# Kernel optimization log

Hardware: AMD Instinct MI355X
Metric: run time of the kernel (lower is better)

Reference implementation:

```python
import jax, jax.numpy as jnp
import numpy as np

N_NODES = 100000
N_EDGES = 1600000
IN_DIM, HID_DIM, OUT_DIM = 128, 128, 64


def setup_inputs() -> dict:
    key = jax.random.key(0)
    ks = jax.random.split(key, 5)
    x = jax.random.normal(ks[0], (N_NODES, IN_DIM), dtype=jnp.float32)
    edge_index = jax.random.randint(ks[1], (2, N_EDGES), 0, N_NODES, dtype=jnp.int64)
    W1 = jax.random.normal(ks[2], (IN_DIM, HID_DIM), dtype=jnp.float32) * (1.0 / np.sqrt(IN_DIM))
    b1 = jnp.zeros((HID_DIM,), dtype=jnp.float32)
    W2 = jax.random.normal(ks[3], (HID_DIM, OUT_DIM), dtype=jnp.float32) * (1.0 / np.sqrt(HID_DIM))
    b2 = jnp.zeros((OUT_DIM,), dtype=jnp.float32)
    return {"x": x, "edge_index": edge_index, "W1": W1, "b1": b1, "W2": W2, "b2": b2}


def _gcn_conv(h, row, col, norm, b, n_nodes):
    # h: [N, F] already linearly transformed; message = norm_e * h[src]; scatter-add to dst
    msg = h[row] * norm[:, None]                      # [E+N, F]
    out = jax.ops.segment_sum(msg, col, num_segments=n_nodes)
    return out + b


def reference(x, edge_index, W1, b1, W2, b2):
    n = x.shape[0]
    loops = jnp.arange(n, dtype=edge_index.dtype)
    row = jnp.concatenate([edge_index[0], loops])     # sources (incl. self loops)
    col = jnp.concatenate([edge_index[1], loops])     # targets
    # symmetric normalization: deg over targets with unit edge weights
    deg = jax.ops.segment_sum(jnp.ones_like(col, dtype=x.dtype), col, num_segments=n)
    dinv = jnp.where(deg > 0, jax.lax.rsqrt(jnp.maximum(deg, 1.0)), 0.0)
    norm = dinv[row] * dinv[col]                      # [E+N]
    h = jax.nn.relu(_gcn_conv(x @ W1, row, col, norm, b1, n))
    out = _gcn_conv(h @ W2, row, col, norm, b2, n)
    return out.mean(axis=0)                           # [OUT_DIM]
```

## Files before the change

### kernel.cpp

```cpp
#include <hip/hip_runtime.h>

#define N_NODES 100000
#define N_EDGES 1600000
#define IN_DIM 128
#define HID_DIM 128
#define OUT_DIM 64
#define BKT_SHIFT 8
#define BKT_SIZE 256
#define NBKT ((N_NODES + BKT_SIZE - 1) / BKT_SIZE)
#define B1 256
#define HIST_N (NBKT * B1)
#define HIST_N2 (2 * HIST_N)
#define GEMM_BLKS ((N_NODES + 127) / 128)

typedef float v2f __attribute__((ext_vector_type(2)));
typedef float v4f __attribute__((ext_vector_type(4)));
typedef short v8s __attribute__((ext_vector_type(8)));

__device__ __forceinline__ unsigned int f2bf(float f) {
  unsigned int u = __float_as_uint(f);
  return (u + 0x7FFFu + ((u >> 16) & 1u)) >> 16;
}

__device__ __forceinline__ void load4(const void* ei, int is64, int half, int base,
                                      int* v) {
  if (is64) {
    const long long* e = (const long long*)ei + (size_t)half * N_EDGES + base;
    longlong2 a = *(const longlong2*)e;
    longlong2 b = *(const longlong2*)(e + 2);
    v[0] = (int)a.x; v[1] = (int)a.y; v[2] = (int)b.x; v[3] = (int)b.y;
  } else {
    const int* e = (const int*)ei + (size_t)half * N_EDGES + base;
    int4 a = *(const int4*)e;
    v[0] = a.x; v[1] = a.y; v[2] = a.z; v[3] = a.w;
  }
}

__device__ __forceinline__ int detect64_block(const unsigned int* ei, int* sh) {
  if (threadIdx.x == 0) *sh = 0;
  __syncthreads();
  if (ei[1 + 2 * threadIdx.x] != 0u) *sh = 1;
  __syncthreads();
  return (*sh == 0) ? 1 : 0;
}

__global__ __launch_bounds__(256) void front_kernel(const float* __restrict__ x,
                                                    const float* __restrict__ W,
                                                    const void* ei,
                                                    unsigned int* __restrict__ G,
                                                    int* hist, float* S) {
  __shared__ __align__(16) char smem[2 * 128 * 136 * 2];
  if (blockIdx.x >= GEMM_BLKS) {
    int* hd = (int*)smem;
    int* hs = hd + NBKT;
    int* sh = hs + NBKT;
    const int hb = blockIdx.x - GEMM_BLKS;
    if (hb == 0 && threadIdx.x < HID_DIM) S[threadIdx.x] = 0.f;
    const int is64 = detect64_block((const unsigned int*)ei, sh);
    for (int k = threadIdx.x; k < NBKT; k += 256) { hd[k] = 0; hs[k] = 0; }
    __syncthreads();
    for (int g = hb * 256 + threadIdx.x; g < N_EDGES / 4; g += B1 * 256) {
      int r[4], c[4];
      load4(ei, is64, 0, g * 4, r);
      load4(ei, is64, 1, g * 4, c);
#pragma unroll
      for (int k = 0; k < 4; k++) {
        atomicAdd(&hd[c[k] >> BKT_SHIFT], 1);
        atomicAdd(&hs[r[k] >> BKT_SHIFT], 1);
      }
    }
    __syncthreads();
    for (int k = threadIdx.x; k < NBKT; k += 256) {
      hist[k * B1 + hb] = hd[k];
      hist[HIST_N + k * B1 + hb] = hs[k];
    }
    return;
  }
  typedef unsigned short us_row[136];
  us_row* lx = (us_row*)smem;
  us_row* lwt = (us_row*)(smem + 128 * 136 * 2);
  const int t = threadIdx.x;
  const int row0 = blockIdx.x * 128;

  {
    const float4* W4 = (const float4*)W;
    for (int it = 0; it < 16; ++it) {
      int idx = t + 256 * it;
      int k = idx >> 5, c4 = (idx & 31) * 4;
      float4 w = W4[idx];
      lwt[c4 + 0][k] = (unsigned short)f2bf(w.x);
      lwt[c4 + 1][k] = (unsigned short)f2bf(w.y);
      lwt[c4 + 2][k] = (unsigned short)f2bf(w.z);
      lwt[c4 + 3][k] = (unsigned short)f2bf(w.w);
    }
  }
  {
    const float4* x4 = (const float4*)(x + (size_t)row0 * IN_DIM);
    for (int it = 0; it < 16; ++it) {
      int idx = t + 256 * it;
      int r = idx >> 5, kq = (idx & 31) * 4;
      float4 v = make_float4(0.f, 0.f, 0.f, 0.f);
      if (row0 + r < N_NODES) v = x4[idx];
      unsigned int p0 = (f2bf(v.y) << 16) | f2bf(v.x);
      unsigned int p1 = (f2bf(v.w) << 16) | f2bf(v.z);
      *(uint2*)&lx[r][kq] = make_uint2(p0, p1);
    }
  }
  __syncthreads();

  const int lane = t & 63;
  const int wv = t >> 6;
  const int m0 = wv * 32;
  const int lrow = lane & 15;
  const int lk = (lane >> 4) * 8;

  v4f acc[2][8];
#pragma unroll
  for (int si = 0; si < 2; si++)
#pragma unroll
    for (int n = 0; n < 8; n++) acc[si][n] = (v4f){0.f, 0.f, 0.f, 0.f};

#pragma unroll
  for (int kk = 0; kk < 128; kk += 32) {
    v8s a0 = *(const v8s*)&lx[m0 + lrow][kk + lk];
    v8s a1 = *(const v8s*)&lx[m0 + 16 + lrow][kk + lk];
#pragma unroll
    for (int n = 0; n < 8; n++) {
      v8s b = *(const v8s*)&lwt[n * 16 + lrow][kk + lk];
      acc[0][n] = __builtin_amdgcn_mfma_f32_16x16x32_bf16(a0, b, acc[0][n], 0, 0, 0);
      acc[1][n] = __builtin_amdgcn_mfma_f32_16x16x32_bf16(a1, b, acc[1][n], 0, 0, 0);
    }
  }

  unsigned char* G8 = (unsigned char*)G;
#pragma unroll
  for (int si = 0; si < 2; si++)
#pragma unroll
    for (int n = 0; n < 8; n++) {
      int colg = n * 16 + (lane & 15);
#pragma unroll
      for (int i = 0; i < 4; i++) {
        int r = row0 + m0 + si * 16 + (lane >> 4) * 4 + i;
        if (r < N_NODES) {
          float v = acc[si][n][i];
          int pk = __builtin_amdgcn_cvt_pk_fp8_f32(v, v, 0, false);
          G8[(size_t)r * HID_DIM + colg] = (unsigned char)(pk & 0xFF);
        }
      }
    }
}

__global__ void scan1_kernel(int* arr, int* bsum, int n) {
  __shared__ int tmp[256];
  int i = blockIdx.x * 256 + threadIdx.x;
  int v = (i < n) ? arr[i] : 0;
  tmp[threadIdx.x] = v;
  __syncthreads();
  for (int off = 1; off < 256; off <<= 1) {
    int t2 = (threadIdx.x >= off) ? tmp[threadIdx.x - off] : 0;
    __syncthreads();
    tmp[threadIdx.x] += t2;
    __syncthreads();
  }
  if (i < n) arr[i] = tmp[threadIdx.x] - v;
  if (threadIdx.x == 255) bsum[blockIdx.x] = tmp[255];
}

__global__ void scan2_kernel(int* bsum, int nb) {
  __shared__ int tmp[1024];
  int v = (threadIdx.x < nb) ? bsum[threadIdx.x] : 0;
  tmp[threadIdx.x] = v;
  __syncthreads();
  for (int off = 1; off < 1024; off <<= 1) {
    int t2 = (threadIdx.x >= off) ? tmp[threadIdx.x - off] : 0;
    __syncthreads();
    tmp[threadIdx.x] += t2;
    __syncthreads();
  }
  if (threadIdx.x < nb) bsum[threadIdx.x] = tmp[threadIdx.x] - v;
}

__global__ __launch_bounds__(256) void scatter_kernel(const void* ei, const int* hist,
                                                      const int* bsum,
                                                      unsigned int* pairs) {
  __shared__ int cd[NBKT], cs[NBKT], sh[1];
  const int is64 = detect64_block((const unsigned int*)ei, sh);
  for (int k = threadIdx.x; k < NBKT; k += 256) {
    cd[k] = hist[k * B1 + blockIdx.x] + bsum[k];
    cs[k] = hist[HIST_N + k * B1 + blockIdx.x] + bsum[NBKT + k];
  }
  __syncthreads();
  for (int g = blockIdx.x * 256 + threadIdx.x; g < N_EDGES / 4; g += B1 * 256) {
    int r[4], c[4];
    load4(ei, is64, 0, g * 4, r);
    load4(ei, is64, 1, g * 4, c);
#pragma unroll
    for (int k = 0; k < 4; k++) {
      int pd = atomicAdd(&cd[c[k] >> BKT_SHIFT], 1);
      pairs[pd] = ((unsigned int)(c[k] & (BKT_SIZE - 1)) << 17) | (unsigned int)r[k];
      int ps = atomicAdd(&cs[r[k] >> BKT_SHIFT], 1);
      pairs[ps] = ((unsigned int)(r[k] & (BKT_SIZE - 1)) << 17) | (unsigned int)c[k];
    }
  }
}

__global__ __launch_bounds__(256) void csr_kernel(const int* hist, const int* bsum,
                                                  const unsigned int* pairs,
                                                  int* rowptr, int* csr, float* dinv) {
  __shared__ int cnt[BKT_SIZE], sc[BKT_SIZE], cur[BKT_SIZE];
  const int k = blockIdx.x;
  const int base = hist[k * B1] + bsum[k];
  const int end = (k == NBKT - 1) ? N_EDGES : hist[(k + 1) * B1] + bsum[k + 1];
  const int nseg = end - base;
  const int l = threadIdx.x;
  cnt[l] = 0;
  __syncthreads();
  for (int i = l; i < nseg; i += 256) atomicAdd(&cnt[pairs[base + i] >> 17], 1);
  __syncthreads();
  sc[l] = cnt[l];
  __syncthreads();
  for (int off = 1; off < BKT_SIZE; off <<= 1) {
    int v = (l >= off) ? sc[l - off] : 0;
    __syncthreads();
    sc[l] += v;
    __syncthreads();
  }
  {
    int excl = sc[l] - cnt[l];
    cur[l] = base + excl;
    int v = k * BKT_SIZE + l;
    if (v < N_NODES) {
      rowptr[v] = base + excl;
      dinv[v] = rsqrtf((float)(cnt[l] + 1));
    }
  }
  if (k == NBKT - 1 && l == 0) rowptr[N_NODES] = N_EDGES;
  __syncthreads();
  for (int i = l; i < nseg; i += 256) {
    unsigned int pk = pairs[base + i];
    int pos = atomicAdd(&cur[pk >> 17], 1);
    csr[pos] = (int)(pk & 0x1FFFFu);
  }
}

__global__ __launch_bounds__(256) void outsum_kernel(const int* hist, const int* bsum,
                                                     const unsigned int* pairs,
                                                     const float* __restrict__ dinv,
                                                     float* wacc) {
  __shared__ float fb[BKT_SIZE];
  const int k = blockIdx.x;
  const int base = hist[HIST_N + k * B1] + bsum[NBKT + k];
  const int end =
      (k == NBKT - 1) ? 2 * N_EDGES : hist[HIST_N + (k + 1) * B1] + bsum[NBKT + k + 1];
  fb[threadIdx.x] = 0.f;
  __syncthreads();
  for (int i = base + threadIdx.x; i < end; i += 256) {
    unsigned int pk = pairs[i];
    atomicAdd(&fb[pk >> 17], dinv[pk & 0x1FFFFu]);
  }
  __syncthreads();
  int v = k * BKT_SIZE + threadIdx.x;
  if (v < N_NODES) wacc[v] = fb[threadIdx.x];
}

__global__ __launch_bounds__(256) void aggregate_kernel(
    const unsigned int* __restrict__ G, const int* __restrict__ rowptr,
    const int* __restrict__ csr, const float* __restrict__ dinv,
    const float* __restrict__ wacc, const float* __restrict__ b1,
    float* __restrict__ S) {
  const int lane = threadIdx.x & 63;
  const int sub = lane & 31;
  const int half = lane >> 5;
  const int wid = blockIdx.x * (blockDim.x >> 6) + (threadIdx.x >> 6);
  const int nwaves = gridDim.x * (blockDim.x >> 6);
  const float4 b = ((const float4*)b1)[sub];
  v2f s01 = {0.f, 0.f}, s23 = {0.f, 0.f};

  for (int c = wid; c < N_NODES; c += nwaves) {
    const int start = rowptr[c];
    const int cnum = rowptr[c + 1] - start;
    float d = 0.f;
    v2f a01 = {0.f, 0.f}, a23 = {0.f, 0.f};
    if (half == 0) {
      d = dinv[c];
      unsigned int g = G[c * 32 + sub];
      a01 = __builtin_amdgcn_cvt_pk_f32_fp8((int)g, false) * d;
      a23 = __builtin_amdgcn_cvt_pk_f32_fp8((int)g, true) * d;
    }
    for (int j0 = 0; j0 < cnum; j0 += 64) {
      int src = 0;
      float dvl = 0.f;
      if (j0 + lane < cnum) {
        src = __builtin_nontemporal_load(&csr[start + j0 + lane]);
        dvl = dinv[src];
      }
      const int m = min(64, cnum - j0);
      int i = 0;
      for (; i + 16 <= m; i += 16) {
        int s0 = __shfl(src, i + half);
        int s1 = __shfl(src, i + 2 + half);
        int s2 = __shfl(src, i + 4 + half);
        int s3 = __shfl(src, i + 6 + half);
        int s4 = __shfl(src, i + 8 + half);
        int s5 = __shfl(src, i + 10 + half);
        int s6 = __shfl(src, i + 12 + half);
        int s7 = __shfl(src, i + 14 + half);
        float w0 = __shfl(dvl, i + half);
        float w1 = __shfl(dvl, i + 2 + half);
        float w2 = __shfl(dvl, i + 4 + half);
        float w3 = __shfl(dvl, i + 6 + half);
        float w4 = __shfl(dvl, i + 8 + half);
        float w5 = __shfl(dvl, i + 10 + half);
        float w6 = __shfl(dvl, i + 12 + half);
        float w7 = __shfl(dvl, i + 14 + half);
        unsigned int g0 = G[s0 * 32 + sub];
        unsigned int g1 = G[s1 * 32 + sub];
        unsigned int g2 = G[s2 * 32 + sub];
        unsigned int g3 = G[s3 * 32 + sub];
        unsigned int g4 = G[s4 * 32 + sub];
        unsigned int g5 = G[s5 * 32 + sub];
        unsigned int g6 = G[s6 * 32 + sub];
        unsigned int g7 = G[s7 * 32 + sub];
        a01 += __builtin_amdgcn_cvt_pk_f32_fp8((int)g0, false) * w0;
        a23 += __builtin_amdgcn_cvt_pk_f32_fp8((int)g0, true) * w0;
        a01 += __builtin_amdgcn_cvt_pk_f32_fp8((int)g1, false) * w1;
        a23 += __builtin_amdgcn_cvt_pk_f32_fp8((int)g1, true) * w1;
        a01 += __builtin_amdgcn_cvt_pk_f32_fp8((int)g2, false) * w2;
        a23 += __builtin_amdgcn_cvt_pk_f32_fp8((int)g2, true) * w2;
        a01 += __builtin_amdgcn_cvt_pk_f32_fp8((int)g3, false) * w3;
        a23 += __builtin_amdgcn_cvt_pk_f32_fp8((int)g3, true) * w3;
        a01 += __builtin_amdgcn_cvt_pk_f32_fp8((int)g4, false) * w4;
        a23 += __builtin_amdgcn_cvt_pk_f32_fp8((int)g4, true) * w4;
        a01 += __builtin_amdgcn_cvt_pk_f32_fp8((int)g5, false) * w5;
        a23 += __builtin_amdgcn_cvt_pk_f32_fp8((int)g5, true) * w5;
        a01 += __builtin_amdgcn_cvt_pk_f32_fp8((int)g6, false) * w6;
        a23 += __builtin_amdgcn_cvt_pk_f32_fp8((int)g6, true) * w6;
        a01 += __builtin_amdgcn_cvt_pk_f32_fp8((int)g7, false) * w7;
        a23 += __builtin_amdgcn_cvt_pk_f32_fp8((int)g7, true) * w7;
      }
      for (; i + 2 <= m; i += 2) {
        int s = __shfl(src, i + half);
        float w = __shfl(dvl, i + half);
        unsigned int g = G[s * 32 + sub];
        a01 += __builtin_amdgcn_cvt_pk_f32_fp8((int)g, false) * w;
        a23 += __builtin_amdgcn_cvt_pk_f32_fp8((int)g, true) * w;
      }
      if (i < m) {
        int s = __shfl(src, i);
        float w = __shfl(dvl, i);
        if (half == 0) {
          unsigned int g = G[s * 32 + sub];
          a01 += __builtin_amdgcn_cvt_pk_f32_fp8((int)g, false) * w;
          a23 += __builtin_amdgcn_cvt_pk_f32_fp8((int)g, true) * w;
        }
      }
    }
    a01.x += __shfl(a01.x, sub + 32);
    a01.y += __shfl(a01.y, sub + 32);
    a23.x += __shfl(a23.x, sub + 32);
    a23.y += __shfl(a23.y, sub + 32);
    if (half == 0) {
      float wc = d * (wacc[c] + d);
      s01.x += wc * fmaxf(fmaf(d, a01.x, b.x), 0.f);
      s01.y += wc * fmaxf(fmaf(d, a01.y, b.y), 0.f);
      s23.x += wc * fmaxf(fmaf(d, a23.x, b.z), 0.f);
      s23.y += wc * fmaxf(fmaf(d, a23.y, b.w), 0.f);
    }
  }

  __shared__ float ls[HID_DIM];
  if (threadIdx.x < HID_DIM) ls[threadIdx.x] = 0.f;
  __syncthreads();
  if (half == 0) {
    atomicAdd(&ls[4 * sub + 0], s01.x);
    atomicAdd(&ls[4 * sub + 1], s01.y);
    atomicAdd(&ls[4 * sub + 2], s23.x);
    atomicAdd(&ls[4 * sub + 3], s23.y);
  }
  __syncthreads();
  if (threadIdx.x < HID_DIM) atomicAdd(&S[threadIdx.x], ls[threadIdx.x]);
}

__global__ void finish_kernel(const float* __restrict__ S, const float* __restrict__ W2,
                              const float* __restrict__ b2, float* __restrict__ out) {
  int j = threadIdx.x;
  float acc = 0.f;
  for (int k = 0; k < HID_DIM; k++) acc += S[k] * W2[k * OUT_DIM + j];
  out[j] = acc * (1.0f / N_NODES) + b2[j];
}

extern "C" void kernel_launch(void* const* d_in, const int* in_sizes, int n_in,
                              void* d_out, int out_size, void* d_ws, size_t ws_size,
                              hipStream_t stream) {
  const float* x  = (const float*)d_in[0];
  const void*  ei = d_in[1];
  const float* W1 = (const float*)d_in[2];
  const float* b1 = (const float*)d_in[3];
  const float* W2 = (const float*)d_in[4];
  const float* b2 = (const float*)d_in[5];
  float* out = (float*)d_out;

  char* p = (char*)d_ws;
  size_t off = 0;
  auto alloc = [&](size_t bytes) -> void* {
    void* r = p + off;
    off = (off + bytes + 63) & ~(size_t)63;
    return r;
  };
  int*   hist   = (int*)alloc((size_t)HIST_N2 * 4);
  int*   bsum   = (int*)alloc(1024 * 4);
  unsigned int* pairs = (unsigned int*)alloc((size_t)2 * N_EDGES * 4);
  int*   rowptr = (int*)alloc(((size_t)N_NODES + 1) * 4);
  int*   csr    = (int*)alloc((size_t)N_EDGES * 4);
  float* dinv   = (float*)alloc((size_t)N_NODES * 4);
  float* wacc   = (float*)alloc((size_t)N_NODES * 4);
  float* S      = (float*)alloc(HID_DIM * 4);
  unsigned int* G = (unsigned int*)alloc((size_t)N_NODES * HID_DIM);
  (void)ws_size; (void)n_in; (void)in_sizes; (void)out_size;

  const int NBH = HIST_N2 / 256;

  front_kernel<<<GEMM_BLKS + B1, 256, 0, stream>>>(x, W1, ei, G, hist, S);
  scan1_kernel<<<NBH, 256, 0, stream>>>(hist, bsum, HIST_N2);
  scan2_kernel<<<1, 1024, 0, stream>>>(bsum, NBH);
  scatter_kernel<<<B1, 256, 0, stream>>>(ei, hist, bsum, pairs);
  csr_kernel<<<NBKT, 256, 0, stream>>>(hist, bsum, pairs, rowptr, csr, dinv);
  outsum_kernel<<<NBKT, 256, 0, stream>>>(hist, bsum, pairs, dinv, wacc);
  aggregate_kernel<<<2048, 256, 0, stream>>>(G, rowptr, csr, dinv, wacc, b1, S);
  finish_kernel<<<1, 64, 0, stream>>>(S, W2, b2, out);
}
```

Measured before the change: 298.4 us.

## Prescale fp8 features by source dinv in outsum to drop per-edge weights

The outsum kernel now multiplies each node's fp8 feature row by its own dinv and re-quantizes it to fp8 in place. The aggregate kernel therefore sums raw gathered values, with no per-edge dinv gather or weight shuffle, and applies the destination dinv once per node. The inner unroll drops from 16 to 8 edges. Storing the scaled values back in fp8 adds a second rounding, which costs some accuracy, and outsum gains an extra read-modify-write pass over G.

```diff
diff --git a/kernel.cpp b/kernel.cpp
--- a/kernel.cpp
+++ b/kernel.cpp
@@ -246,7 +246,8 @@
 __global__ __launch_bounds__(256) void outsum_kernel(const int* hist, const int* bsum,
                                                      const unsigned int* pairs,
                                                      const float* __restrict__ dinv,
-                                                     float* wacc) {
+                                                     float* wacc,
+                                                     unsigned int* __restrict__ G) {
   __shared__ float fb[BKT_SIZE];
   const int k = blockIdx.x;
   const int base = hist[HIST_N + k * B1] + bsum[NBKT + k];
@@ -257,6 +258,23 @@
   for (int i = base + threadIdx.x; i < end; i += 256) {
     unsigned int pk = pairs[i];
     atomicAdd(&fb[pk >> 17], dinv[pk & 0x1FFFFu]);
+  }
+  {
+    const int j0 = k * BKT_SIZE * 32;
+#pragma unroll
+    for (int it = 0; it < 32; ++it) {
+      int j = j0 + it * 256 + threadIdx.x;
+      int node = j >> 5;
+      if (node < N_NODES) {
+        float d = dinv[node];
+        unsigned int g = G[j];
+        v2f lo = __builtin_amdgcn_cvt_pk_f32_fp8((int)g, false) * d;
+        v2f hi = __builtin_amdgcn_cvt_pk_f32_fp8((int)g, true) * d;
+        int pk2 = __builtin_amdgcn_cvt_pk_fp8_f32(lo.x, lo.y, 0, false);
+        pk2 = __builtin_amdgcn_cvt_pk_fp8_f32(hi.x, hi.y, pk2, true);
+        G[j] = (unsigned int)pk2;
+      }
+    }
   }
   __syncthreads();
   int v = k * BKT_SIZE + threadIdx.x;
@@ -279,79 +297,48 @@
   for (int c = wid; c < N_NODES; c += nwaves) {
     const int start = rowptr[c];
     const int cnum = rowptr[c + 1] - start;
-    float d = 0.f;
     v2f a01 = {0.f, 0.f}, a23 = {0.f, 0.f};
     if (half == 0) {
-      d = dinv[c];
       unsigned int g = G[c * 32 + sub];
-      a01 = __builtin_amdgcn_cvt_pk_f32_fp8((int)g, false) * d;
-      a23 = __builtin_amdgcn_cvt_pk_f32_fp8((int)g, true) * d;
+      a01 = __builtin_amdgcn_cvt_pk_f32_fp8((int)g, false);
+      a23 = __builtin_amdgcn_cvt_pk_f32_fp8((int)g, true);
     }
     for (int j0 = 0; j0 < cnum; j0 += 64) {
       int src = 0;
-      float dvl = 0.f;
-      if (j0 + lane < cnum) {
+      if (j0 + lane < cnum)
         src = __builtin_nontemporal_load(&csr[start + j0 + lane]);
-        dvl = dinv[src];
-      }
       const int m = min(64, cnum - j0);
       int i = 0;
-      for (; i + 16 <= m; i += 16) {
+      for (; i + 8 <= m; i += 8) {
         int s0 = __shfl(src, i + half);
         int s1 = __shfl(src, i + 2 + half);
         int s2 = __shfl(src, i + 4 + half);
         int s3 = __shfl(src, i + 6 + half);
-        int s4 = __shfl(src, i + 8 + half);
-        int s5 = __shfl(src, i + 10 + half);
-        int s6 = __shfl(src, i + 12 + half);
-        int s7 = __shfl(src, i + 14 + half);
-        float w0 = __shfl(dvl, i + half);
-        float w1 = __shfl(dvl, i + 2 + half);
-        float w2 = __shfl(dvl, i + 4 + half);
-        float w3 = __shfl(dvl, i + 6 + half);
-        float w4 = __shfl(dvl, i + 8 + half);
-        float w5 = __shfl(dvl, i + 10 + half);
-        float w6 = __shfl(dvl, i + 12 + half);
-        float w7 = __shfl(dvl, i + 14 + half);
         unsigned int g0 = G[s0 * 32 + sub];
         unsigned int g1 = G[s1 * 32 + sub];
         unsigned int g2 = G[s2 * 32 + sub];
         unsigned int g3 = G[s3 * 32 + sub];
-        unsigned int g4 = G[s4 * 32 + sub];
-        unsigned int g5 = G[s5 * 32 + sub];
-        unsigned int g6 = G[s6 * 32 + sub];
-        unsigned int g7 = G[s7 * 32 + sub];
-        a01 += __builtin_amdgcn_cvt_pk_f32_fp8((int)g0, false) * w0;
-        a23 += __builtin_amdgcn_cvt_pk_f32_fp8((int)g0, true) * w0;
-        a01 += __builtin_amdgcn_cvt_pk_f32_fp8((int)g1, false) * w1;
-        a23 += __builtin_amdgcn_cvt_pk_f32_fp8((int)g1, true) * w1;
-        a01 += __builtin_amdgcn_cvt_pk_f32_fp8((int)g2, false) * w2;
-        a23 += __builtin_amdgcn_cvt_pk_f32_fp8((int)g2, true) * w2;
-        a01 += __builtin_amdgcn_cvt_pk_f32_fp8((int)g3, false) * w3;
-        a23 += __builtin_amdgcn_cvt_pk_f32_fp8((int)g3, true) * w3;
-        a01 += __builtin_amdgcn_cvt_pk_f32_fp8((int)g4, false) * w4;
-        a23 += __builtin_amdgcn_cvt_pk_f32_fp8((int)g4, true) * w4;
-        a01 += __builtin_amdgcn_cvt_pk_f32_fp8((int)g5, false) * w5;
-        a23 += __builtin_amdgcn_cvt_pk_f32_fp8((int)g5, true) * w5;
-        a01 += __builtin_amdgcn_cvt_pk_f32_fp8((int)g6, false) * w6;
-        a23 += __builtin_amdgcn_cvt_pk_f32_fp8((int)g6, true) * w6;
-        a01 += __builtin_amdgcn_cvt_pk_f32_fp8((int)g7, false) * w7;
-        a23 += __builtin_amdgcn_cvt_pk_f32_fp8((int)g7, true) * w7;
+        a01 += __builtin_amdgcn_cvt_pk_f32_fp8((int)g0, false) +
+               __builtin_amdgcn_cvt_pk_f32_fp8((int)g1, false);
+        a23 += __builtin_amdgcn_cvt_pk_f32_fp8((int)g0, true) +
+               __builtin_amdgcn_cvt_pk_f32_fp8((int)g1, true);
+        a01 += __builtin_amdgcn_cvt_pk_f32_fp8((int)g2, false) +
+               __builtin_amdgcn_cvt_pk_f32_fp8((int)g3, false);
+        a23 += __builtin_amdgcn_cvt_pk_f32_fp8((int)g2, true) +
+               __builtin_amdgcn_cvt_pk_f32_fp8((int)g3, true);
       }
       for (; i + 2 <= m; i += 2) {
         int s = __shfl(src, i + half);
-        float w = __shfl(dvl, i + half);
         unsigned int g = G[s * 32 + sub];
-        a01 += __builtin_amdgcn_cvt_pk_f32_fp8((int)g, false) * w;
-        a23 += __builtin_amdgcn_cvt_pk_f32_fp8((int)g, true) * w;
+        a01 += __builtin_amdgcn_cvt_pk_f32_fp8((int)g, false);
+        a23 += __builtin_amdgcn_cvt_pk_f32_fp8((int)g, true);
       }
       if (i < m) {
         int s = __shfl(src, i);
-        float w = __shfl(dvl, i);
         if (half == 0) {
           unsigned int g = G[s * 32 + sub];
-          a01 += __builtin_amdgcn_cvt_pk_f32_fp8((int)g, false) * w;
-          a23 += __builtin_amdgcn_cvt_pk_f32_fp8((int)g, true) * w;
+          a01 += __builtin_amdgcn_cvt_pk_f32_fp8((int)g, false);
+          a23 += __builtin_amdgcn_cvt_pk_f32_fp8((int)g, true);
         }
       }
     }
@@ -360,6 +347,7 @@
     a23.x += __shfl(a23.x, sub + 32);
     a23.y += __shfl(a23.y, sub + 32);
     if (half == 0) {
+      float d = dinv[c];
       float wc = d * (wacc[c] + d);
       s01.x += wc * fmaxf(fmaf(d, a01.x, b.x), 0.f);
       s01.y += wc * fmaxf(fmaf(d, a01.y, b.y), 0.f);
@@ -425,7 +413,7 @@
   scan2_kernel<<<1, 1024, 0, stream>>>(bsum, NBH);
   scatter_kernel<<<B1, 256, 0, stream>>>(ei, hist, bsum, pairs);
   csr_kernel<<<NBKT, 256, 0, stream>>>(hist, bsum, pairs, rowptr, csr, dinv);
-  outsum_kernel<<<NBKT, 256, 0, stream>>>(hist, bsum, pairs, dinv, wacc);
+  outsum_kernel<<<NBKT, 256, 0, stream>>>(hist, bsum, pairs, dinv, wacc, G);
   aggregate_kernel<<<2048, 256, 0, stream>>>(G, rowptr, csr, dinv, wacc, b1, S);
   finish_kernel<<<1, 64, 0, stream>>>(S, W2, b2, out);
 }
```

New measurement: 290.7 us. 1.03x faster.
